# Kernel optimization log

Hardware: AMD Instinct MI355X
Metric: run time of the kernel (lower is better)

Reference implementation:

```python
import jax, jax.numpy as jnp
import numpy as np

H, KVH, D = 32, 8, 128
HID = H * D
OP = H * D + 2 * KVH * D
T = 2048
LAYER_IDX = 8
LAMBDA_INIT = float(0.8 - 0.6 * np.exp(-0.3 * LAYER_IDX))
EPS = 1e-5


def setup_inputs() -> dict:
    key = jax.random.key(0)
    ks = jax.random.split(key, 10)
    s = 0.02
    return {
        "hidden_states": jax.random.normal(ks[0], (T, HID), jnp.float32),
        "wqkv_w": jax.random.normal(ks[1], (OP, HID), jnp.float32) * s,
        "wqkv_b": jax.random.normal(ks[2], (OP,), jnp.float32) * s,
        "lambda_q1": jax.random.normal(ks[3], (D,), jnp.float32) * 0.1,
        "lambda_k1": jax.random.normal(ks[4], (D,), jnp.float32) * 0.1,
        "lambda_q2": jax.random.normal(ks[5], (D,), jnp.float32) * 0.1,
        "lambda_k2": jax.random.normal(ks[6], (D,), jnp.float32) * 0.1,
        "subln_w": jnp.ones((2 * D,), jnp.float32),
        "out_w": jax.random.normal(ks[7], (HID, HID), jnp.float32) * s,
        "out_b": jax.random.normal(ks[8], (HID,), jnp.float32) * s,
    }


def reference(hidden_states, wqkv_w, wqkv_b, lambda_q1, lambda_k1,
              lambda_q2, lambda_k2, subln_w, out_w, out_b):
    t = hidden_states.shape[0]
    scale = D ** -0.5

    qkv = hidden_states @ wqkv_w.T + wqkv_b                     # [T, OP]
    q, k, v = jnp.split(qkv, [H * D, H * D + KVH * D], axis=-1)

    # pair-wise head split: consecutive heads form (pair, component) groups
    q = q.reshape(t, H // 2, 2, D)                              # [T, Hp, 2, D]
    k = k.reshape(t, KVH // 2, 2, D)                            # [T, KVHp, 2, D]
    v = v.reshape(t, KVH // 2, 2 * D)                           # [T, KVHp, 2D]

    rep = H // KVH  # GQA: query pair p -> kv pair p // rep
    k = jnp.repeat(k, rep, axis=1)                              # [T, Hp, 2, D]
    v = jnp.repeat(v, rep, axis=1)                              # [T, Hp, 2D]

    lam = (jnp.exp(jnp.dot(lambda_q1, lambda_k1))
           - jnp.exp(jnp.dot(lambda_q2, lambda_k2)) + LAMBDA_INIT)

    causal = jnp.tril(jnp.ones((t, t), bool))
    scores = jnp.einsum('qhcd,khcd->hcqk', q, k) * scale        # [Hp, 2, T, T]
    scores = jnp.where(causal, scores, -jnp.inf)
    probs = jax.nn.softmax(scores, axis=-1)
    attn = probs[:, 0] - lam * probs[:, 1]                      # [Hp, T, T]

    out = jnp.einsum('hqk,khd->qhd', attn, v)                   # [T, Hp, 2D]

    # per-head RMSNorm over 2D, scaled by (1 - lambda_init)
    rms = jax.lax.rsqrt(jnp.mean(out * out, axis=-1, keepdims=True) + EPS)
    out = out * rms * subln_w * (1.0 - LAMBDA_INIT)

    out = out.reshape(t, H * D)
    return out @ out_w.T + out_b
```

## Files before the change

kernel.cpp:

```cpp
#include <hip/hip_runtime.h>

#define TTOK 2048
#define HIDN 4096
#define OPD  6144
#define DH   128
#define VD   256
#define KOFF 4096
#define VOFF 5120

typedef short  s16x8 __attribute__((ext_vector_type(8)));
typedef unsigned short u16x8 __attribute__((ext_vector_type(8)));
typedef float  fx4   __attribute__((ext_vector_type(4)));

constexpr float LAM_INIT = 0.7455692280263534f;
constexpr float OML      = 1.0f - LAM_INIT;
constexpr float QKSCALE  = 0.08838834764831845f;
constexpr float RESCALE_THR = 8.0f;

__device__ __forceinline__ unsigned short f2bf(float f) {
  unsigned int u = __builtin_bit_cast(unsigned int, f);
  u += 0x7fffu + ((u >> 16) & 1u);
  return (unsigned short)(u >> 16);
}

__device__ __forceinline__ void g2l16(const void* gsrc, void* ldst) {
  __builtin_amdgcn_global_load_lds(
      (const __attribute__((address_space(1))) unsigned int*)gsrc,
      (__attribute__((address_space(3))) unsigned int*)ldst, 16, 0, 0);
}

__global__ __launch_bounds__(256)
void cvt3(const float* __restrict__ s0, unsigned short* __restrict__ d0, int nb0,
          const float* __restrict__ s1, unsigned short* __restrict__ d1, int nb1,
          const float* __restrict__ s2, unsigned short* __restrict__ d2)
{
  const int b = blockIdx.x;
  const float* s; unsigned short* d; int base;
  if (b < nb0)            { s = s0; d = d0; base = b << 11; }
  else if (b < nb0 + nb1) { s = s1; d = d1; base = (b - nb0) << 11; }
  else                    { s = s2; d = d2; base = (b - nb0 - nb1) << 11; }
  const int i = base + (int)threadIdx.x * 8;
  const float4 a0 = *(const float4*)(s + i);
  const float4 a1 = *(const float4*)(s + i + 4);
  u16x8 v;
  v[0]=f2bf(a0.x); v[1]=f2bf(a0.y); v[2]=f2bf(a0.z); v[3]=f2bf(a0.w);
  v[4]=f2bf(a1.x); v[5]=f2bf(a1.y); v[6]=f2bf(a1.z); v[7]=f2bf(a1.w);
  *(u16x8*)(d + i) = v;
}

__global__ __launch_bounds__(256)
void reduce2(const float* __restrict__ p, const float* __restrict__ bias,
             float* __restrict__ out)
{
  const size_t i = ((size_t)blockIdx.x * 256 + threadIdx.x) * 4;
  const int col = (int)(i & (HIDN - 1));
  const float4 a = *(const float4*)(p + i);
  const float4 b = *(const float4*)(p + (size_t)TTOK * HIDN + i);
  const float4 c = *(const float4*)(bias + col);
  float4 r;
  r.x = a.x + b.x + c.x; r.y = a.y + b.y + c.y;
  r.z = a.z + b.z + c.z; r.w = a.w + b.w + c.w;
  *(float4*)(out + i) = r;
}

template<int MW, int MODE>
__global__ __launch_bounds__(512, 2)
void gemm_8ph(const unsigned short* __restrict__ A, const unsigned short* __restrict__ B,
              const float* __restrict__ bias, void* __restrict__ Cp,
              unsigned short* __restrict__ ctt, int K, int lda, int ldb, int ldc)
{
  constexpr int BM   = MW * 32;
  constexpr int MH   = MW / 2;
  constexpr int ALD2 = MW / 4;
  __shared__ __align__(16) unsigned short As[2][2][(BM / 2) * 64];
  __shared__ __align__(16) unsigned short Bs[2][2][128 * 64];

  const int tid  = threadIdx.x;
  const int lane = tid & 63, wid = tid >> 6;
  const int wm = wid >> 2, wn = wid & 3;
  const int m0 = blockIdx.y * BM, n0 = blockIdx.x * 256;
  const int l15 = lane & 15, lg = lane >> 4;
  const int kOff = (MODE == 1) ? blockIdx.z * K : 0;

  const int srow = tid >> 3;
  const int scol = ((tid & 7) ^ ((tid >> 3) & 7)) << 3;
  const int rsw = (l15 & 7) << 3;
  const int ck0 = (lg * 8) ^ rsw;
  const int ck1 = (32 + lg * 8) ^ rsw;
  const int arh = wm * 16 + l15;
  const int brh = wn * 16 + l15;

  auto stageAh = [&](int kt, int buf, int h) {
    #pragma unroll
    for (int i = 0; i < ALD2; ++i)
      g2l16(A + (size_t)(m0 + h * (BM / 2) + i * 64 + srow) * lda + kOff + kt + scol,
            &As[buf][h][(i * 512 + tid) * 8]);
  };
  auto stageBh = [&](int kt, int buf, int h) {
    #pragma unroll
    for (int i = 0; i < 2; ++i)
      g2l16(B + (size_t)(n0 + h * 128 + i * 64 + srow) * ldb + kOff + kt + scol,
            &Bs[buf][h][(i * 512 + tid) * 8]);
  };

  fx4 acc[MW][4] = {};

  const int nk = K >> 6;
  stageAh(0, 0, 0); stageBh(0, 0, 0); stageBh(0, 0, 1); stageAh(0, 0, 1);
  asm volatile("s_waitcnt vmcnt(0)" ::: "memory");
  __builtin_amdgcn_s_barrier();

  for (int t = 0; t < nk; ++t) {
    const int buf = t & 1, nb = buf ^ 1;
    const int kt1 = (t + 1) << 6;
    const bool pre = (t + 1) < nk;
    const unsigned short* A0 = &As[buf][0][0];
    const unsigned short* A1 = &As[buf][1][0];
    const unsigned short* B0 = &Bs[buf][0][0];
    const unsigned short* B1 = &Bs[buf][1][0];
    s16x8 af[MH][2], bf0[2][2], bf1[2][2];

    #pragma unroll
    for (int m = 0; m < MH; ++m) {
      af[m][0] = *(const s16x8*)&A0[(arh + m * 32) * 64 + ck0];
      af[m][1] = *(const s16x8*)&A0[(arh + m * 32) * 64 + ck1];
    }
    #pragma unroll
    for (int n = 0; n < 2; ++n) {
      bf0[n][0] = *(const s16x8*)&B0[(brh + n * 64) * 64 + ck0];
      bf0[n][1] = *(const s16x8*)&B0[(brh + n * 64) * 64 + ck1];
    }
    if (pre) {
      stageAh(kt1, nb, 0);
      asm volatile("s_waitcnt vmcnt(4)" ::: "memory");
    } else {
      asm volatile("s_waitcnt vmcnt(0)" ::: "memory");
    }
    __builtin_amdgcn_s_barrier();
    __builtin_amdgcn_s_setprio(1);
    #pragma unroll
    for (int m = 0; m < MH; ++m)
      #pragma unroll
      for (int n = 0; n < 2; ++n) {
        acc[m][n] = __builtin_amdgcn_mfma_f32_16x16x32_bf16(af[m][0], bf0[n][0], acc[m][n], 0, 0, 0);
        acc[m][n] = __builtin_amdgcn_mfma_f32_16x16x32_bf16(af[m][1], bf0[n][1], acc[m][n], 0, 0, 0);
      }
    __builtin_amdgcn_s_setprio(0);

    #pragma unroll
    for (int n = 0; n < 2; ++n) {
      bf1[n][0] = *(const s16x8*)&B1[(brh + n * 64) * 64 + ck0];
      bf1[n][1] = *(const s16x8*)&B1[(brh + n * 64) * 64 + ck1];
    }
    if (pre) {
      stageBh(kt1, nb, 0);
      asm volatile("s_waitcnt vmcnt(4)" ::: "memory");
    }
    __builtin_amdgcn_s_barrier();
    __builtin_amdgcn_s_setprio(1);
    #pragma unroll
    for (int m = 0; m < MH; ++m)
      #pragma unroll
      for (int n = 0; n < 2; ++n) {
        acc[m][2 + n] = __builtin_amdgcn_mfma_f32_16x16x32_bf16(af[m][0], bf1[n][0], acc[m][2 + n], 0, 0, 0);
        acc[m][2 + n] = __builtin_amdgcn_mfma_f32_16x16x32_bf16(af[m][1], bf1[n][1], acc[m][2 + n], 0, 0, 0);
      }
    __builtin_amdgcn_s_setprio(0);

    #pragma unroll
    for (int m = 0; m < MH; ++m) {
      af[m][0] = *(const s16x8*)&A1[(arh + m * 32) * 64 + ck0];
      af[m][1] = *(const s16x8*)&A1[(arh + m * 32) * 64 + ck1];
    }
    if (pre) stageBh(kt1, nb, 1);
    __builtin_amdgcn_s_setprio(1);
    #pragma unroll
    for (int m = 0; m < MH; ++m)
      #pragma unroll
      for (int n = 0; n < 2; ++n) {
        acc[MH + m][2 + n] = __builtin_amdgcn_mfma_f32_16x16x32_bf16(af[m][0], bf1[n][0], acc[MH + m][2 + n], 0, 0, 0);
        acc[MH + m][2 + n] = __builtin_amdgcn_mfma_f32_16x16x32_bf16(af[m][1], bf1[n][1], acc[MH + m][2 + n], 0, 0, 0);
      }
    __builtin_amdgcn_s_setprio(0);

    if (pre) stageAh(kt1, nb, 1);
    __builtin_amdgcn_s_setprio(1);
    #pragma unroll
    for (int m = 0; m < MH; ++m)
      #pragma unroll
      for (int n = 0; n < 2; ++n) {
        acc[MH + m][n] = __builtin_amdgcn_mfma_f32_16x16x32_bf16(af[m][0], bf0[n][0], acc[MH + m][n], 0, 0, 0);
        acc[MH + m][n] = __builtin_amdgcn_mfma_f32_16x16x32_bf16(af[m][1], bf0[n][1], acc[MH + m][n], 0, 0, 0);
      }
    __builtin_amdgcn_s_setprio(0);
    if (pre) asm volatile("s_waitcnt vmcnt(4)" ::: "memory");
    __builtin_amdgcn_s_barrier();
  }

  const int rb = m0 + wm * 16;
  const int cb = n0 + wn * 16;
  if (MODE == 1) {
    float* P = (float*)Cp + (size_t)blockIdx.z * (size_t)gridDim.y * BM * ldc;
    #pragma unroll
    for (int mi = 0; mi < MW; ++mi)
      #pragma unroll
      for (int ni = 0; ni < 4; ++ni) {
        const int col = cb + ni * 64 + l15;
        const fx4 a = acc[mi][ni];
        #pragma unroll
        for (int jj = 0; jj < 4; ++jj)
          P[(size_t)(rb + mi * 32 + lg * 4 + jj) * ldc + col] = a[jj];
      }
  } else if (n0 >= VOFF) {
    #pragma unroll
    for (int mi = 0; mi < MW; ++mi)
      #pragma unroll
      for (int ni = 0; ni < 4; ++ni) {
        const int col = cb + ni * 64 + l15;
        const float bv = bias[col];
        const fx4 a = acc[mi][ni];
        ushort4 pk;
        pk.x = f2bf(a[0] + bv); pk.y = f2bf(a[1] + bv);
        pk.z = f2bf(a[2] + bv); pk.w = f2bf(a[3] + bv);
        const int d   = col - VOFF;
        const int kvp = d >> 8, dw = d & 255;
        const int row0 = rb + mi * 32 + lg * 4;
        const int kt2 = row0 >> 5, kk = row0 & 31;
        const int kc = kk >> 3, k8 = kk & 7;
        *(ushort4*)&ctt[(size_t)kvp * 1048576 + (size_t)kt2 * 16384 + 8192
                        + kc * 2048 + dw * 8 + k8] = pk;
      }
  } else if (n0 >= KOFF) {
    #pragma unroll
    for (int mi = 0; mi < MW; ++mi)
      #pragma unroll
      for (int ni = 0; ni < 4; ++ni) {
        const int col = cb + ni * 64 + l15;
        const int ccol = col - KOFF;
        const float bv = bias[col];
        const int kvp = ccol >> 8, cw = ccol & 255;
        const int cc = cw >> 3, cbt = cw & 7;
        const fx4 a = acc[mi][ni];
        #pragma unroll
        for (int jj = 0; jj < 4; ++jj) {
          const int row2 = rb + mi * 32 + lg * 4 + jj;
          const int kt2 = row2 >> 5, kk = row2 & 31;
          ctt[(size_t)kvp * 1048576 + (size_t)kt2 * 16384 + cc * 256 + kk * 8 + cbt]
              = f2bf(a[jj] + bv);
        }
      }
  } else {
    #pragma unroll
    for (int mi = 0; mi < MW; ++mi)
      #pragma unroll
      for (int ni = 0; ni < 4; ++ni) {
        const int col = cb + ni * 64 + l15;
        const float bv = bias[col];
        const fx4 a = acc[mi][ni];
        #pragma unroll
        for (int jj = 0; jj < 4; ++jj) {
          const int row2 = rb + mi * 32 + lg * 4 + jj;
          ((unsigned short*)Cp)[(size_t)row2 * ldc + col] = f2bf((a[jj] + bv) * QKSCALE);
        }
      }
  }
}

__global__ __launch_bounds__(256, 2)
void attn_kernel(const unsigned short* __restrict__ qq,
                 const unsigned short* __restrict__ ctt,
                 const float* __restrict__ lq1, const float* __restrict__ lk1,
                 const float* __restrict__ lq2, const float* __restrict__ lk2,
                 const float* __restrict__ subln,
                 unsigned short* __restrict__ attn_out)
{
  __shared__ __align__(16) unsigned short Sb[2][16384];
  __shared__ __align__(16) unsigned short Pl[4][2][640];
  const int tid = threadIdx.x;
  const int lane = tid & 63, w = tid >> 6;
  const int l15 = lane & 15, lg = lane >> 4;

  const int bid  = blockIdx.x;
  const int r    = bid & 255;
  const int pair = r & 15;
  const int x    = r >> 4;
  const int qb   = (bid >> 8) ? x : 31 - x;
  const int kvp  = pair >> 2;
  const int q0b  = qb * 64;
  const int q0w  = q0b + w * 16;
  const int nt   = 2 * qb + 2;

  const unsigned short* cbase = ctt + (size_t)kvp * 1048576;

  auto stage = [&](int kt, int buf) {
    const unsigned short* src = cbase + (size_t)kt * 16384;
    const int off = w * 512 + lane * 8;
    #pragma unroll
    for (int i = 0; i < 8; ++i) {
      const int o = i * 2048 + off;
      g2l16(src + o, &Sb[buf][o]);
    }
  };

  stage(0, 0);

  float a1 = lq1[lane] * lk1[lane] + lq1[lane + 64] * lk1[lane + 64];
  float a2 = lq2[lane] * lk2[lane] + lq2[lane + 64] * lk2[lane + 64];
  #pragma unroll
  for (int sft = 1; sft < 64; sft <<= 1) { a1 += __shfl_xor(a1, sft); a2 += __shfl_xor(a2, sft); }
  const float lam = __expf(a1) - __expf(a2) + LAM_INIT;

  s16x8 qf0[4], qf1[4];
  {
    const unsigned short* qbp = qq + (size_t)(q0w + l15) * HIDN + pair * VD + lg * 8;
    #pragma unroll
    for (int kf = 0; kf < 4; ++kf) {
      qf0[kf] = *(const s16x8*)(qbp + kf * 32);
      qf1[kf] = *(const s16x8*)(qbp + DH + kf * 32);
    }
  }

  float mrun0 = -1e30f, mrun1 = -1e30f;
  float lrun0 = 0.f, lrun1 = 0.f;
  fx4 oacc0[16] = {}, oacc1[16] = {};
  unsigned short* pl0 = &Pl[w][0][0];
  unsigned short* pl1 = &Pl[w][1][0];
  const int q = q0w + l15;
  const int qmax = q0w + 15;

  for (int t = 0; t < nt; ++t) {
    __syncthreads();
    if (t + 1 < nt) stage(t + 1, (t + 1) & 1);
    const int kb = t * 32;
    if (kb > qmax) continue;
    const unsigned short* Kl = Sb[t & 1];
    const unsigned short* Vl = Sb[t & 1] + 8192;

    fx4 s00 = {0,0,0,0}, s01 = {0,0,0,0}, s10 = {0,0,0,0}, s11 = {0,0,0,0};
    #pragma unroll
    for (int kf = 0; kf < 4; ++kf) {
      const int cc0 = kf * 4 + lg;
      const int cc1 = 16 + kf * 4 + lg;
      const s16x8 k00 = *(const s16x8*)&Kl[cc0 * 256 + l15 * 8];
      const s16x8 k01 = *(const s16x8*)&Kl[cc0 * 256 + (16 + l15) * 8];
      const s16x8 k10 = *(const s16x8*)&Kl[cc1 * 256 + l15 * 8];
      const s16x8 k11 = *(const s16x8*)&Kl[cc1 * 256 + (16 + l15) * 8];
      s00 = __builtin_amdgcn_mfma_f32_16x16x32_bf16(k00, qf0[kf], s00, 0, 0, 0);
      s01 = __builtin_amdgcn_mfma_f32_16x16x32_bf16(k01, qf0[kf], s01, 0, 0, 0);
      s10 = __builtin_amdgcn_mfma_f32_16x16x32_bf16(k10, qf1[kf], s10, 0, 0, 0);
      s11 = __builtin_amdgcn_mfma_f32_16x16x32_bf16(k11, qf1[kf], s11, 0, 0, 0);
    }

    float v0[8], v1[8];
    if (kb + 32 <= q0w) {
      #pragma unroll
      for (int j = 0; j < 4; ++j) {
        v0[j] = s00[j]; v0[4 + j] = s01[j];
        v1[j] = s10[j]; v1[4 + j] = s11[j];
      }
    } else {
      #pragma unroll
      for (int j = 0; j < 4; ++j) {
        const int klo = kb + lg * 4 + j, khi = klo + 16;
        v0[j]     = (klo <= q) ? s00[j] : -1e30f;
        v0[4 + j] = (khi <= q) ? s01[j] : -1e30f;
        v1[j]     = (klo <= q) ? s10[j] : -1e30f;
        v1[4 + j] = (khi <= q) ? s11[j] : -1e30f;
      }
    }
    float tm0 = fmaxf(fmaxf(fmaxf(v0[0],v0[1]),fmaxf(v0[2],v0[3])),
                      fmaxf(fmaxf(v0[4],v0[5]),fmaxf(v0[6],v0[7])));
    float tm1 = fmaxf(fmaxf(fmaxf(v1[0],v1[1]),fmaxf(v1[2],v1[3])),
                      fmaxf(fmaxf(v1[4],v1[5]),fmaxf(v1[6],v1[7])));
    tm0 = fmaxf(tm0, __shfl_xor(tm0, 16)); tm0 = fmaxf(tm0, __shfl_xor(tm0, 32));
    tm1 = fmaxf(tm1, __shfl_xor(tm1, 16)); tm1 = fmaxf(tm1, __shfl_xor(tm1, 32));

    const bool need = (tm0 > mrun0 + RESCALE_THR) || (tm1 > mrun1 + RESCALE_THR);
    if (__any(need)) {
      const float mn0 = fmaxf(mrun0, tm0), mn1 = fmaxf(mrun1, tm1);
      const float fac0 = __expf(mrun0 - mn0), fac1 = __expf(mrun1 - mn1);
      mrun0 = mn0; mrun1 = mn1;
      lrun0 *= fac0; lrun1 *= fac1;
      #pragma unroll
      for (int jj = 0; jj < 4; ++jj) {
        const float fr0 = __shfl(fac0, lg * 4 + jj);
        const float fr1 = __shfl(fac1, lg * 4 + jj);
        #pragma unroll
        for (int nf = 0; nf < 16; ++nf) { oacc0[nf][jj] *= fr0; oacc1[nf][jj] *= fr1; }
      }
    }

    {
      float ps0 = 0.f, ps1 = 0.f;
      ushort4 lo0, hi0, lo1, hi1;
      float p;
      p = __expf(v0[0]-mrun0); ps0 += p; lo0.x = f2bf(p);
      p = __expf(v0[1]-mrun0); ps0 += p; lo0.y = f2bf(p);
      p = __expf(v0[2]-mrun0); ps0 += p; lo0.z = f2bf(p);
      p = __expf(v0[3]-mrun0); ps0 += p; lo0.w = f2bf(p);
      p = __expf(v0[4]-mrun0); ps0 += p; hi0.x = f2bf(p);
      p = __expf(v0[5]-mrun0); ps0 += p; hi0.y = f2bf(p);
      p = __expf(v0[6]-mrun0); ps0 += p; hi0.z = f2bf(p);
      p = __expf(v0[7]-mrun0); ps0 += p; hi0.w = f2bf(p);
      p = __expf(v1[0]-mrun1); ps1 += p; lo1.x = f2bf(p);
      p = __expf(v1[1]-mrun1); ps1 += p; lo1.y = f2bf(p);
      p = __expf(v1[2]-mrun1); ps1 += p; lo1.z = f2bf(p);
      p = __expf(v1[3]-mrun1); ps1 += p; lo1.w = f2bf(p);
      p = __expf(v1[4]-mrun1); ps1 += p; hi1.x = f2bf(p);
      p = __expf(v1[5]-mrun1); ps1 += p; hi1.y = f2bf(p);
      p = __expf(v1[6]-mrun1); ps1 += p; hi1.z = f2bf(p);
      p = __expf(v1[7]-mrun1); ps1 += p; hi1.w = f2bf(p);
      lrun0 += ps0; lrun1 += ps1;
      *(ushort4*)&pl0[l15 * 40 + lg * 4]      = lo0;
      *(ushort4*)&pl0[l15 * 40 + 16 + lg * 4] = hi0;
      *(ushort4*)&pl1[l15 * 40 + lg * 4]      = lo1;
      *(ushort4*)&pl1[l15 * 40 + 16 + lg * 4] = hi1;
    }
    asm volatile("s_waitcnt lgkmcnt(0)" ::: "memory");
    __builtin_amdgcn_sched_barrier(0);

    const s16x8 pa0 = *(const s16x8*)&pl0[l15 * 40 + lg * 8];
    const s16x8 pa1 = *(const s16x8*)&pl1[l15 * 40 + lg * 8];
    #pragma unroll
    for (int nf = 0; nf < 16; ++nf) {
      const s16x8 vf = *(const s16x8*)&Vl[lg * 2048 + (nf * 16 + l15) * 8];
      oacc0[nf] = __builtin_amdgcn_mfma_f32_16x16x32_bf16(pa0, vf, oacc0[nf], 0, 0, 0);
      oacc1[nf] = __builtin_amdgcn_mfma_f32_16x16x32_bf16(pa1, vf, oacc1[nf], 0, 0, 0);
    }
  }

  lrun0 += __shfl_xor(lrun0, 16); lrun0 += __shfl_xor(lrun0, 32);
  lrun1 += __shfl_xor(lrun1, 16); lrun1 += __shfl_xor(lrun1, 32);

  float li0[4], li1[4];
  #pragma unroll
  for (int jj = 0; jj < 4; ++jj) {
    li0[jj] = 1.0f / __shfl(lrun0, lg * 4 + jj);
    li1[jj] = 1.0f / __shfl(lrun1, lg * 4 + jj);
  }

  float ss[4] = {0.f, 0.f, 0.f, 0.f};
  #pragma unroll
  for (int nf = 0; nf < 16; ++nf)
    #pragma unroll
    for (int jj = 0; jj < 4; ++jj) {
      const float o = oacc0[nf][jj] * li0[jj] - lam * oacc1[nf][jj] * li1[jj];
      oacc0[nf][jj] = o;
      ss[jj] += o * o;
    }
  #pragma unroll
  for (int jj = 0; jj < 4; ++jj) {
    ss[jj] += __shfl_xor(ss[jj], 1);
    ss[jj] += __shfl_xor(ss[jj], 2);
    ss[jj] += __shfl_xor(ss[jj], 4);
    ss[jj] += __shfl_xor(ss[jj], 8);
    ss[jj] = rsqrtf(ss[jj] * (1.0f / 256.0f) + 1e-5f) * OML;
  }
  #pragma unroll
  for (int nf = 0; nf < 16; ++nf) {
    const int dcol = nf * 16 + l15;
    const float sw = subln[dcol];
    #pragma unroll
    for (int jj = 0; jj < 4; ++jj) {
      const int t = q0w + lg * 4 + jj;
      attn_out[(size_t)t * HIDN + pair * VD + dcol] = f2bf(oacc0[nf][jj] * ss[jj] * sw);
    }
  }
}

extern "C" void kernel_launch(void* const* d_in, const int* in_sizes, int n_in,
                              void* d_out, int out_size, void* d_ws, size_t ws_size,
                              hipStream_t stream) {
  (void)in_sizes; (void)n_in; (void)out_size; (void)ws_size;
  const float* hs     = (const float*)d_in[0];
  const float* wqkv_w = (const float*)d_in[1];
  const float* wqkv_b = (const float*)d_in[2];
  const float* lq1    = (const float*)d_in[3];
  const float* lk1    = (const float*)d_in[4];
  const float* lq2    = (const float*)d_in[5];
  const float* lk2    = (const float*)d_in[6];
  const float* subln  = (const float*)d_in[7];
  const float* out_w  = (const float*)d_in[8];
  const float* out_b  = (const float*)d_in[9];

  unsigned short* qq       = (unsigned short*)d_ws;
  unsigned short* ctt      = qq + (size_t)TTOK * HIDN;
  unsigned short* attn_out = ctt + (size_t)4 * 1048576;
  unsigned short* hs_bf    = attn_out + (size_t)TTOK * HIDN;
  unsigned short* wqkv_bf  = hs_bf + (size_t)TTOK * HIDN;
  unsigned short* outw_bf  = wqkv_bf + (size_t)OPD * HIDN;
  float*          partial  = (float*)hs_bf;

  const int nb0 = (TTOK * HIDN) >> 11;
  const int nb1 = (OPD * HIDN) >> 11;
  const int nb2 = (HIDN * HIDN) >> 11;
  cvt3<<<dim3(nb0 + nb1 + nb2), 256, 0, stream>>>(
      hs, hs_bf, nb0, wqkv_w, wqkv_bf, nb1, out_w, outw_bf);

  gemm_8ph<8, 0><<<dim3(OPD / 256, TTOK / 256), 512, 0, stream>>>(
      hs_bf, wqkv_bf, wqkv_b, qq, ctt, HIDN, HIDN, HIDN, HIDN);

  attn_kernel<<<dim3(512), 256, 0, stream>>>(
      qq, ctt, lq1, lk1, lq2, lk2, subln, attn_out);

  gemm_8ph<8, 1><<<dim3(HIDN / 256, TTOK / 256, 2), 512, 0, stream>>>(
      attn_out, outw_bf, nullptr, partial, nullptr, HIDN / 2, HIDN, HIDN, HIDN);

  reduce2<<<dim3((TTOK * HIDN) / 1024), 256, 0, stream>>>(
      partial, out_b, (float*)d_out);
}
```

Baseline: 330.7 us.

## Retile QKV projection GEMM to 256x192 tiles with new warp layout

The QKV projection GEMM is split into its own kernel using 256x192 output tiles, which gives 32x8=256 blocks instead of 24x8=192. Warps are rearranged as 4x2, each computing 4x6 MFMA fragments, and the B tile is staged in one 192-row buffer. The aim is to fill the device's compute units better and reduce the tail of partially used waves. The epilogue now picks the Q, K or V output path per 16-column fragment rather than per block, which adds branches. The out-projection GEMM is de-templated into a dedicated split-K kernel with the same 256x256 tiling.

```diff
diff --git a/kernel.cpp b/kernel.cpp
--- a/kernel.cpp
+++ b/kernel.cpp
@@ -63,26 +63,169 @@
   *(float4*)(out + i) = r;
 }
 
-template<int MW, int MODE>
 __global__ __launch_bounds__(512, 2)
-void gemm_8ph(const unsigned short* __restrict__ A, const unsigned short* __restrict__ B,
-              const float* __restrict__ bias, void* __restrict__ Cp,
-              unsigned short* __restrict__ ctt, int K, int lda, int ldb, int ldc)
+void gemm1_qkv(const unsigned short* __restrict__ A, const unsigned short* __restrict__ B,
+               const float* __restrict__ bias, unsigned short* __restrict__ qq,
+               unsigned short* __restrict__ ctt)
 {
-  constexpr int BM   = MW * 32;
-  constexpr int MH   = MW / 2;
-  constexpr int ALD2 = MW / 4;
-  __shared__ __align__(16) unsigned short As[2][2][(BM / 2) * 64];
+  __shared__ __align__(16) unsigned short As[2][2][128 * 64];
+  __shared__ __align__(16) unsigned short Bs[2][192 * 64];
+
+  const int tid  = threadIdx.x;
+  const int lane = tid & 63, wid = tid >> 6;
+  const int wm = wid >> 1, wn = wid & 1;
+  const int m0 = blockIdx.y * 256, n0 = blockIdx.x * 192;
+  const int l15 = lane & 15, lg = lane >> 4;
+
+  const int scol = ((tid & 7) ^ ((tid >> 3) & 7)) << 3;
+  const int rsw = (l15 & 7) << 3;
+  const int ck0 = (lg * 8) ^ rsw;
+  const int ck1 = (32 + lg * 8) ^ rsw;
+  const int arh = wm * 16 + l15;
+  const int brh = wn * 96 + l15;
+
+  auto stageAh = [&](int kt, int buf, int h) {
+    #pragma unroll
+    for (int i = 0; i < 2; ++i) {
+      const int li = i * 512 + tid;
+      g2l16(A + (size_t)(m0 + h * 128 + (li >> 3)) * HIDN + kt + scol,
+            &As[buf][h][li * 8]);
+    }
+  };
+  auto stageB = [&](int kt, int buf) {
+    #pragma unroll
+    for (int i = 0; i < 3; ++i) {
+      const int li = i * 512 + tid;
+      g2l16(B + (size_t)(n0 + (li >> 3)) * HIDN + kt + scol,
+            &Bs[buf][li * 8]);
+    }
+  };
+
+  fx4 acc[4][6] = {};
+
+  const int nk = HIDN >> 6;
+  stageAh(0, 0, 0); stageB(0, 0); stageAh(0, 0, 1);
+  asm volatile("s_waitcnt vmcnt(0)" ::: "memory");
+  __builtin_amdgcn_s_barrier();
+
+  for (int t = 0; t < nk; ++t) {
+    const int buf = t & 1, nb = buf ^ 1;
+    const int kt1 = (t + 1) << 6;
+    const bool pre = (t + 1) < nk;
+    const unsigned short* A0 = &As[buf][0][0];
+    const unsigned short* A1 = &As[buf][1][0];
+    const unsigned short* Bp = &Bs[buf][0];
+    s16x8 af[2], bk0[6], bk1[6];
+
+    af[0] = *(const s16x8*)&A0[(arh)      * 64 + ck0];
+    af[1] = *(const s16x8*)&A0[(arh + 64) * 64 + ck0];
+    #pragma unroll
+    for (int n = 0; n < 6; ++n)
+      bk0[n] = *(const s16x8*)&Bp[(brh + n * 16) * 64 + ck0];
+    if (pre) {
+      stageAh(kt1, nb, 0);
+      asm volatile("s_waitcnt vmcnt(2)" ::: "memory");
+    } else {
+      asm volatile("s_waitcnt vmcnt(0)" ::: "memory");
+    }
+    __builtin_amdgcn_s_barrier();
+    __builtin_amdgcn_s_setprio(1);
+    #pragma unroll
+    for (int m = 0; m < 2; ++m)
+      #pragma unroll
+      for (int n = 0; n < 6; ++n)
+        acc[m][n] = __builtin_amdgcn_mfma_f32_16x16x32_bf16(af[m], bk0[n], acc[m][n], 0, 0, 0);
+    __builtin_amdgcn_s_setprio(0);
+
+    af[0] = *(const s16x8*)&A0[(arh)      * 64 + ck1];
+    af[1] = *(const s16x8*)&A0[(arh + 64) * 64 + ck1];
+    #pragma unroll
+    for (int n = 0; n < 6; ++n)
+      bk1[n] = *(const s16x8*)&Bp[(brh + n * 16) * 64 + ck1];
+    if (pre) stageB(kt1, nb);
+    __builtin_amdgcn_s_barrier();
+    __builtin_amdgcn_s_setprio(1);
+    #pragma unroll
+    for (int m = 0; m < 2; ++m)
+      #pragma unroll
+      for (int n = 0; n < 6; ++n)
+        acc[m][n] = __builtin_amdgcn_mfma_f32_16x16x32_bf16(af[m], bk1[n], acc[m][n], 0, 0, 0);
+    __builtin_amdgcn_s_setprio(0);
+
+    af[0] = *(const s16x8*)&A1[(arh)      * 64 + ck0];
+    af[1] = *(const s16x8*)&A1[(arh + 64) * 64 + ck0];
+    if (pre) stageAh(kt1, nb, 1);
+    __builtin_amdgcn_s_setprio(1);
+    #pragma unroll
+    for (int m = 0; m < 2; ++m)
+      #pragma unroll
+      for (int n = 0; n < 6; ++n)
+        acc[2 + m][n] = __builtin_amdgcn_mfma_f32_16x16x32_bf16(af[m], bk0[n], acc[2 + m][n], 0, 0, 0);
+    __builtin_amdgcn_s_setprio(0);
+
+    af[0] = *(const s16x8*)&A1[(arh)      * 64 + ck1];
+    af[1] = *(const s16x8*)&A1[(arh + 64) * 64 + ck1];
+    __builtin_amdgcn_s_setprio(1);
+    #pragma unroll
+    for (int m = 0; m < 2; ++m)
+      #pragma unroll
+      for (int n = 0; n < 6; ++n)
+        acc[2 + m][n] = __builtin_amdgcn_mfma_f32_16x16x32_bf16(af[m], bk1[n], acc[2 + m][n], 0, 0, 0);
+    __builtin_amdgcn_s_setprio(0);
+  }
+
+  #pragma unroll
+  for (int mi = 0; mi < 4; ++mi)
+    #pragma unroll
+    for (int ni = 0; ni < 6; ++ni) {
+      const int colg = n0 + wn * 96 + ni * 16;
+      const int col  = colg + l15;
+      const float bv = bias[col];
+      const fx4 a = acc[mi][ni];
+      const int row0 = m0 + mi * 64 + wm * 16 + lg * 4;
+      if (colg >= VOFF) {
+        ushort4 pk;
+        pk.x = f2bf(a[0] + bv); pk.y = f2bf(a[1] + bv);
+        pk.z = f2bf(a[2] + bv); pk.w = f2bf(a[3] + bv);
+        const int d = col - VOFF;
+        const int kvp = d >> 8, dw = d & 255;
+        const int kt2 = row0 >> 5, kk = row0 & 31;
+        const int kc = kk >> 3, k8 = kk & 7;
+        *(ushort4*)&ctt[(size_t)kvp * 1048576 + (size_t)kt2 * 16384 + 8192
+                        + kc * 2048 + dw * 8 + k8] = pk;
+      } else if (colg >= KOFF) {
+        const int ccol = col - KOFF;
+        const int kvp = ccol >> 8, cw = ccol & 255;
+        const int cc = cw >> 3, cbt = cw & 7;
+        #pragma unroll
+        for (int jj = 0; jj < 4; ++jj) {
+          const int row2 = row0 + jj;
+          const int kt2 = row2 >> 5, kk = row2 & 31;
+          ctt[(size_t)kvp * 1048576 + (size_t)kt2 * 16384 + cc * 256 + kk * 8 + cbt]
+              = f2bf(a[jj] + bv);
+        }
+      } else {
+        #pragma unroll
+        for (int jj = 0; jj < 4; ++jj)
+          qq[(size_t)(row0 + jj) * HIDN + col] = f2bf((a[jj] + bv) * QKSCALE);
+      }
+    }
+}
+
+__global__ __launch_bounds__(512, 2)
+void gemm2_sk(const unsigned short* __restrict__ A, const unsigned short* __restrict__ B,
+              float* __restrict__ P, int K, int lda, int ldb, int ldc)
+{
+  __shared__ __align__(16) unsigned short As[2][2][128 * 64];
   __shared__ __align__(16) unsigned short Bs[2][2][128 * 64];
 
   const int tid  = threadIdx.x;
   const int lane = tid & 63, wid = tid >> 6;
   const int wm = wid >> 2, wn = wid & 3;
-  const int m0 = blockIdx.y * BM, n0 = blockIdx.x * 256;
+  const int m0 = blockIdx.y * 256, n0 = blockIdx.x * 256;
   const int l15 = lane & 15, lg = lane >> 4;
-  const int kOff = (MODE == 1) ? blockIdx.z * K : 0;
-
-  const int srow = tid >> 3;
+  const int kOff = blockIdx.z * K;
+
   const int scol = ((tid & 7) ^ ((tid >> 3) & 7)) << 3;
   const int rsw = (l15 & 7) << 3;
   const int ck0 = (lg * 8) ^ rsw;
@@ -92,18 +235,22 @@
 
   auto stageAh = [&](int kt, int buf, int h) {
     #pragma unroll
-    for (int i = 0; i < ALD2; ++i)
-      g2l16(A + (size_t)(m0 + h * (BM / 2) + i * 64 + srow) * lda + kOff + kt + scol,
-            &As[buf][h][(i * 512 + tid) * 8]);
+    for (int i = 0; i < 2; ++i) {
+      const int li = i * 512 + tid;
+      g2l16(A + (size_t)(m0 + h * 128 + (li >> 3)) * lda + kOff + kt + scol,
+            &As[buf][h][li * 8]);
+    }
   };
   auto stageBh = [&](int kt, int buf, int h) {
     #pragma unroll
-    for (int i = 0; i < 2; ++i)
-      g2l16(B + (size_t)(n0 + h * 128 + i * 64 + srow) * ldb + kOff + kt + scol,
-            &Bs[buf][h][(i * 512 + tid) * 8]);
+    for (int i = 0; i < 2; ++i) {
+      const int li = i * 512 + tid;
+      g2l16(B + (size_t)(n0 + h * 128 + (li >> 3)) * ldb + kOff + kt + scol,
+            &Bs[buf][h][li * 8]);
+    }
   };
 
-  fx4 acc[MW][4] = {};
+  fx4 acc[8][4] = {};
 
   const int nk = K >> 6;
   stageAh(0, 0, 0); stageBh(0, 0, 0); stageBh(0, 0, 1); stageAh(0, 0, 1);
@@ -118,10 +265,10 @@
     const unsigned short* A1 = &As[buf][1][0];
     const unsigned short* B0 = &Bs[buf][0][0];
     const unsigned short* B1 = &Bs[buf][1][0];
-    s16x8 af[MH][2], bf0[2][2], bf1[2][2];
-
-    #pragma unroll
-    for (int m = 0; m < MH; ++m) {
+    s16x8 af[4][2], bf0[2][2], bf1[2][2];
+
+    #pragma unroll
+    for (int m = 0; m < 4; ++m) {
       af[m][0] = *(const s16x8*)&A0[(arh + m * 32) * 64 + ck0];
       af[m][1] = *(const s16x8*)&A0[(arh + m * 32) * 64 + ck1];
     }
@@ -139,7 +286,7 @@
     __builtin_amdgcn_s_barrier();
     __builtin_amdgcn_s_setprio(1);
     #pragma unroll
-    for (int m = 0; m < MH; ++m)
+    for (int m = 0; m < 4; ++m)
       #pragma unroll
       for (int n = 0; n < 2; ++n) {
         acc[m][n] = __builtin_amdgcn_mfma_f32_16x16x32_bf16(af[m][0], bf0[n][0], acc[m][n], 0, 0, 0);
@@ -159,7 +306,7 @@
     __builtin_amdgcn_s_barrier();
     __builtin_amdgcn_s_setprio(1);
     #pragma unroll
-    for (int m = 0; m < MH; ++m)
+    for (int m = 0; m < 4; ++m)
       #pragma unroll
       for (int n = 0; n < 2; ++n) {
         acc[m][2 + n] = __builtin_amdgcn_mfma_f32_16x16x32_bf16(af[m][0], bf1[n][0], acc[m][2 + n], 0, 0, 0);
@@ -168,102 +315,48 @@
     __builtin_amdgcn_s_setprio(0);
 
     #pragma unroll
-    for (int m = 0; m < MH; ++m) {
+    for (int m = 0; m < 4; ++m) {
       af[m][0] = *(const s16x8*)&A1[(arh + m * 32) * 64 + ck0];
       af[m][1] = *(const s16x8*)&A1[(arh + m * 32) * 64 + ck1];
     }
     if (pre) stageBh(kt1, nb, 1);
     __builtin_amdgcn_s_setprio(1);
     #pragma unroll
-    for (int m = 0; m < MH; ++m)
+    for (int m = 0; m < 4; ++m)
       #pragma unroll
       for (int n = 0; n < 2; ++n) {
-        acc[MH + m][2 + n] = __builtin_amdgcn_mfma_f32_16x16x32_bf16(af[m][0], bf1[n][0], acc[MH + m][2 + n], 0, 0, 0);
-        acc[MH + m][2 + n] = __builtin_amdgcn_mfma_f32_16x16x32_bf16(af[m][1], bf1[n][1], acc[MH + m][2 + n], 0, 0, 0);
+        acc[4 + m][2 + n] = __builtin_amdgcn_mfma_f32_16x16x32_bf16(af[m][0], bf1[n][0], acc[4 + m][2 + n], 0, 0, 0);
+        acc[4 + m][2 + n] = __builtin_amdgcn_mfma_f32_16x16x32_bf16(af[m][1], bf1[n][1], acc[4 + m][2 + n], 0, 0, 0);
       }
     __builtin_amdgcn_s_setprio(0);
 
     if (pre) stageAh(kt1, nb, 1);
     __builtin_amdgcn_s_setprio(1);
     #pragma unroll
-    for (int m = 0; m < MH; ++m)
+    for (int m = 0; m < 4; ++m)
       #pragma unroll
       for (int n = 0; n < 2; ++n) {
-        acc[MH + m][n] = __builtin_amdgcn_mfma_f32_16x16x32_bf16(af[m][0], bf0[n][0], acc[MH + m][n], 0, 0, 0);
-        acc[MH + m][n] = __builtin_amdgcn_mfma_f32_16x16x32_bf16(af[m][1], bf0[n][1], acc[MH + m][n], 0, 0, 0);
+        acc[4 + m][n] = __builtin_amdgcn_mfma_f32_16x16x32_bf16(af[m][0], bf0[n][0], acc[4 + m][n], 0, 0, 0);
+        acc[4 + m][n] = __builtin_amdgcn_mfma_f32_16x16x32_bf16(af[m][1], bf0[n][1], acc[4 + m][n], 0, 0, 0);
       }
     __builtin_amdgcn_s_setprio(0);
     if (pre) asm volatile("s_waitcnt vmcnt(4)" ::: "memory");
     __builtin_amdgcn_s_barrier();
   }
 
+  float* Pz = P + (size_t)blockIdx.z * TTOK * ldc;
   const int rb = m0 + wm * 16;
   const int cb = n0 + wn * 16;
-  if (MODE == 1) {
-    float* P = (float*)Cp + (size_t)blockIdx.z * (size_t)gridDim.y * BM * ldc;
-    #pragma unroll
-    for (int mi = 0; mi < MW; ++mi)
-      #pragma unroll
-      for (int ni = 0; ni < 4; ++ni) {
-        const int col = cb + ni * 64 + l15;
-        const fx4 a = acc[mi][ni];
-        #pragma unroll
-        for (int jj = 0; jj < 4; ++jj)
-          P[(size_t)(rb + mi * 32 + lg * 4 + jj) * ldc + col] = a[jj];
-      }
-  } else if (n0 >= VOFF) {
-    #pragma unroll
-    for (int mi = 0; mi < MW; ++mi)
-      #pragma unroll
-      for (int ni = 0; ni < 4; ++ni) {
-        const int col = cb + ni * 64 + l15;
-        const float bv = bias[col];
-        const fx4 a = acc[mi][ni];
-        ushort4 pk;
-        pk.x = f2bf(a[0] + bv); pk.y = f2bf(a[1] + bv);
-        pk.z = f2bf(a[2] + bv); pk.w = f2bf(a[3] + bv);
-        const int d   = col - VOFF;
-        const int kvp = d >> 8, dw = d & 255;
-        const int row0 = rb + mi * 32 + lg * 4;
-        const int kt2 = row0 >> 5, kk = row0 & 31;
-        const int kc = kk >> 3, k8 = kk & 7;
-        *(ushort4*)&ctt[(size_t)kvp * 1048576 + (size_t)kt2 * 16384 + 8192
-                        + kc * 2048 + dw * 8 + k8] = pk;
-      }
-  } else if (n0 >= KOFF) {
-    #pragma unroll
-    for (int mi = 0; mi < MW; ++mi)
-      #pragma unroll
-      for (int ni = 0; ni < 4; ++ni) {
-        const int col = cb + ni * 64 + l15;
-        const int ccol = col - KOFF;
-        const float bv = bias[col];
-        const int kvp = ccol >> 8, cw = ccol & 255;
-        const int cc = cw >> 3, cbt = cw & 7;
-        const fx4 a = acc[mi][ni];
-        #pragma unroll
-        for (int jj = 0; jj < 4; ++jj) {
-          const int row2 = rb + mi * 32 + lg * 4 + jj;
-          const int kt2 = row2 >> 5, kk = row2 & 31;
-          ctt[(size_t)kvp * 1048576 + (size_t)kt2 * 16384 + cc * 256 + kk * 8 + cbt]
-              = f2bf(a[jj] + bv);
-        }
-      }
-  } else {
-    #pragma unroll
-    for (int mi = 0; mi < MW; ++mi)
-      #pragma unroll
-      for (int ni = 0; ni < 4; ++ni) {
-        const int col = cb + ni * 64 + l15;
-        const float bv = bias[col];
-        const fx4 a = acc[mi][ni];
-        #pragma unroll
-        for (int jj = 0; jj < 4; ++jj) {
-          const int row2 = rb + mi * 32 + lg * 4 + jj;
-          ((unsigned short*)Cp)[(size_t)row2 * ldc + col] = f2bf((a[jj] + bv) * QKSCALE);
-        }
-      }
-  }
+  #pragma unroll
+  for (int mi = 0; mi < 8; ++mi)
+    #pragma unroll
+    for (int ni = 0; ni < 4; ++ni) {
+      const int col = cb + ni * 64 + l15;
+      const fx4 a = acc[mi][ni];
+      #pragma unroll
+      for (int jj = 0; jj < 4; ++jj)
+        Pz[(size_t)(rb + mi * 32 + lg * 4 + jj) * ldc + col] = a[jj];
+    }
 }
 
 __global__ __launch_bounds__(256, 2)
@@ -497,14 +590,14 @@
   cvt3<<<dim3(nb0 + nb1 + nb2), 256, 0, stream>>>(
       hs, hs_bf, nb0, wqkv_w, wqkv_bf, nb1, out_w, outw_bf);
 
-  gemm_8ph<8, 0><<<dim3(OPD / 256, TTOK / 256), 512, 0, stream>>>(
-      hs_bf, wqkv_bf, wqkv_b, qq, ctt, HIDN, HIDN, HIDN, HIDN);
+  gemm1_qkv<<<dim3(OPD / 192, TTOK / 256), 512, 0, stream>>>(
+      hs_bf, wqkv_bf, wqkv_b, qq, ctt);
 
   attn_kernel<<<dim3(512), 256, 0, stream>>>(
       qq, ctt, lq1, lk1, lq2, lk2, subln, attn_out);
 
-  gemm_8ph<8, 1><<<dim3(HIDN / 256, TTOK / 256, 2), 512, 0, stream>>>(
-      attn_out, outw_bf, nullptr, partial, nullptr, HIDN / 2, HIDN, HIDN, HIDN);
+  gemm2_sk<<<dim3(HIDN / 256, TTOK / 256, 2), 512, 0, stream>>>(
+      attn_out, outw_bf, partial, HIDN / 2, HIDN, HIDN, HIDN);
 
   reduce2<<<dim3((TTOK * HIDN) / 1024), 256, 0, stream>>>(
       partial, out_b, (float*)d_out);
```

New measurement: 331.1 us. Within noise of the previous version (+0.1%).
